# Optimization experiments

Hardware: AMD Instinct MI355X
Metric: run time of the kernel (lower is better)

## Reference

```python
import jax, jax.numpy as jnp
import numpy as np

DIM_X = 128
DIM_Z = 128
DIM_IN = DIM_X + DIM_Z   # LSTM units == input width in this model
UNITS = DIM_IN
BATCH = 256
SEQ_LEN = 1024


def setup_inputs() -> dict:
    key = jax.random.key(0)
    ks = jax.random.split(key, 9)
    s = 0.05
    inputs = jax.random.normal(ks[0], (BATCH, SEQ_LEN, DIM_X), jnp.float32)
    # Keras LSTMCell params: kernel [dim_in, 4*units], recurrent_kernel [units, 4*units], bias [4*units]
    kernel = jax.random.normal(ks[1], (DIM_IN, 4 * UNITS), jnp.float32) * s
    recurrent_kernel = jax.random.normal(ks[2], (UNITS, 4 * UNITS), jnp.float32) * s
    bias = jax.random.normal(ks[3], (4 * UNITS,), jnp.float32) * s
    # Gaussian heads
    w_mu = jax.random.normal(ks[4], (UNITS, DIM_Z), jnp.float32) * s
    b_mu = jnp.zeros((DIM_Z,), jnp.float32)
    w_sigma = jax.random.normal(ks[5], (UNITS, DIM_Z), jnp.float32) * s
    b_sigma = jnp.zeros((DIM_Z,), jnp.float32)
    eps = jax.random.normal(ks[6], (SEQ_LEN - 1, BATCH, DIM_Z), jnp.float32)
    return {"inputs": inputs, "kernel": kernel, "recurrent_kernel": recurrent_kernel,
            "bias": bias, "w_mu": w_mu, "b_mu": b_mu, "w_sigma": w_sigma,
            "b_sigma": b_sigma, "eps": eps}


def reference(inputs, kernel, recurrent_kernel, bias, w_mu, b_mu, w_sigma, b_sigma, eps):
    B = inputs.shape[0]

    def cell(h, c, zx):
        # Keras gate order: i, f, g(candidate), o
        gates = zx @ kernel + h @ recurrent_kernel + bias
        i, f, g, o = jnp.split(gates, 4, axis=-1)
        c = jax.nn.sigmoid(f) * c + jax.nn.sigmoid(i) * jnp.tanh(g)
        h = jax.nn.sigmoid(o) * jnp.tanh(c)
        return h, c

    def heads(h):
        mu = h @ w_mu + b_mu
        sigma = jax.nn.softplus(h @ w_sigma + b_sigma) + 1e-6
        return mu, sigma

    # warmup: z = zeros, x = inputs[:, 0, :], zero LSTM state
    h0 = jnp.zeros((B, UNITS), inputs.dtype)
    c0 = jnp.zeros((B, UNITS), inputs.dtype)
    z0 = jnp.zeros((B, DIM_Z), inputs.dtype)
    h, c = cell(h0, c0, jnp.concatenate([z0, inputs[:, 0, :]], axis=-1))
    mu0, sigma0 = heads(h)

    xs = (jnp.swapaxes(inputs[:, 1:, :], 0, 1), eps)  # [T-1, B, dim_x], [T-1, B, dim_z]

    def step(carry, x_eps):
        h, c, mu, sigma = carry
        x, e = x_eps
        z = mu + sigma * e  # reparameterized sample
        h, c = cell(h, c, jnp.concatenate([z, x], axis=-1))
        mu, sigma = heads(h)
        return (h, c, mu, sigma), (mu, sigma)

    _, (mus, sigmas) = jax.lax.scan(step, (h, c, mu0, sigma0), xs)
    mu_preds = jnp.swapaxes(jnp.concatenate([mu0[None], mus], axis=0), 0, 1)      # [B, T, dim_z]
    sigma_preds = jnp.swapaxes(jnp.concatenate([sigma0[None], sigmas], axis=0), 0, 1)
    return (mu_preds, sigma_preds)
```

## Files before the change

### kernel.cpp

```cpp
#include <hip/hip_runtime.h>
#include <hip/hip_bf16.h>
#include <math.h>


#define BATCH 256
#define SEQT  1024
#define DX    128
#define DZ    128
#define UNITS 256
#define G4    1024

__device__ __forceinline__ float ldf(const float* p) { return *p; }
__device__ __forceinline__ float ldf(const __hip_bfloat16* p) { return __bfloat162float(*p); }
__device__ __forceinline__ void stf(float* p, float v) { *p = v; }
__device__ __forceinline__ void stf(__hip_bfloat16* p, float v) { *p = __float2bfloat16(v); }

__device__ __forceinline__ float sigmoidf_(float x) { return 1.0f / (1.0f + expf(-x)); }
__device__ __forceinline__ float softplusf_(float x) {
    float ax = fabsf(x);
    return fmaxf(x, 0.0f) + log1pf(expf(-ax));
}

__global__ void detect_dtype_kernel(const unsigned short* __restrict__ bias_words,
                                    int* __restrict__ flag) {
    __shared__ int any_big;
    if (threadIdx.x == 0) any_big = 0;
    __syncthreads();
    int local = 0;
    for (int i = threadIdx.x; i < 1024; i += 256) {
        unsigned short w = bias_words[i];
        int e = (w >> 7) & 0xFF;
        if (e >= 127) local = 1;
    }
    if (local) atomicOr(&any_big, 1);
    __syncthreads();
    if (threadIdx.x == 0) flag[0] = any_big;
}

template <typename T>
__global__ __launch_bounds__(256) void lstm_ar_kernel(
    const int* __restrict__ flag, int want,
    const T* __restrict__ inp,
    const T* __restrict__ K,
    const T* __restrict__ R,
    const T* __restrict__ bias,
    const T* __restrict__ Wmu,
    const T* __restrict__ bmu,
    const T* __restrict__ Wsig,
    const T* __restrict__ bsig,
    const T* __restrict__ eps,
    T* __restrict__ out)
{
    if (flag[0] != want) return;

    const int b = blockIdx.x;
    const int u = threadIdx.x;

    __shared__ float zx_s[256];
    __shared__ float h_s[256];
    __shared__ float mu_s[128];
    __shared__ float sg_s[128];

    float c = 0.0f;

    const float b_i = ldf(bias + u);
    const float b_f = ldf(bias + 256 + u);
    const float b_g = ldf(bias + 512 + u);
    const float b_o = ldf(bias + 768 + u);
    const float b_head = (u < 128) ? ldf(bmu + u) : ldf(bsig + (u - 128));

    zx_s[u] = 0.0f;
    h_s[u] = 0.0f;
    __syncthreads();
    if (u < 128) {
        zx_s[128 + u] = ldf(inp + ((size_t)b * SEQT + 0) * DX + u);
    }
    __syncthreads();

    const size_t out_sig_off = (size_t)BATCH * SEQT * DZ;

    for (int t = 0; t < SEQT; ++t) {
        float ai = b_i, af = b_f, ag = b_g, ao = b_o;
        {
            const T* kp = K + u;
            #pragma unroll 8
            for (int i = 0; i < 256; ++i) {
                const float a = zx_s[i];
                ai += a * ldf(kp);
                af += a * ldf(kp + 256);
                ag += a * ldf(kp + 512);
                ao += a * ldf(kp + 768);
                kp += G4;
            }
        }
        {
            const T* rp = R + u;
            #pragma unroll 8
            for (int i = 0; i < 256; ++i) {
                const float a = h_s[i];
                ai += a * ldf(rp);
                af += a * ldf(rp + 256);
                ag += a * ldf(rp + 512);
                ao += a * ldf(rp + 768);
                rp += G4;
            }
        }

        const float gi = sigmoidf_(ai);
        const float gf = sigmoidf_(af);
        const float gg = tanhf(ag);
        const float go = sigmoidf_(ao);
        c = gf * c + gi * gg;
        const float hn = go * tanhf(c);

        __syncthreads();
        h_s[u] = hn;
        __syncthreads();

        float acc = b_head;
        if (u < 128) {
            const T* wp = Wmu + u;
            #pragma unroll 8
            for (int k = 0; k < 256; ++k) {
                acc += h_s[k] * ldf(wp);
                wp += DZ;
            }
            mu_s[u] = acc;
            stf(out + ((size_t)b * SEQT + t) * DZ + u, acc);
        } else {
            const int d = u - 128;
            const T* wp = Wsig + d;
            #pragma unroll 8
            for (int k = 0; k < 256; ++k) {
                acc += h_s[k] * ldf(wp);
                wp += DZ;
            }
            const float sg = softplusf_(acc) + 1e-6f;
            sg_s[d] = sg;
            stf(out + out_sig_off + ((size_t)b * SEQT + t) * DZ + d, sg);
        }
        __syncthreads();

        if (t < SEQT - 1) {
            if (u < 128) {
                const float e = ldf(eps + ((size_t)t * BATCH + b) * DZ + u);
                zx_s[u] = mu_s[u] + sg_s[u] * e;
                zx_s[128 + u] = ldf(inp + ((size_t)b * SEQT + (t + 1)) * DX + u);
            }
        }
        __syncthreads();
    }
}

template <typename T>
static void launch_main(const int* flag, int want, void* const* d_in, void* d_out,
                        hipStream_t stream) {
    lstm_ar_kernel<T><<<BATCH, 256, 0, stream>>>(
        flag, want,
        (const T*)d_in[0], (const T*)d_in[1], (const T*)d_in[2], (const T*)d_in[3],
        (const T*)d_in[4], (const T*)d_in[5], (const T*)d_in[6], (const T*)d_in[7],
        (const T*)d_in[8], (T*)d_out);
}

extern "C" void kernel_launch(void* const* d_in, const int* in_sizes, int n_in,
                              void* d_out, int out_size, void* d_ws, size_t ws_size,
                              hipStream_t stream) {
    int* flag = (int*)d_ws;
    detect_dtype_kernel<<<1, 256, 0, stream>>>((const unsigned short*)d_in[3], flag);
    launch_main<__hip_bfloat16>(flag, 0, d_in, d_out, stream);
    launch_main<float>(flag, 1, d_in, d_out, stream);
}
```

Baseline: 23.76 ms.

## Split LSTM weights across persistent blocks with LDS-resident slices and flag-based exchange

Replaces the one-block-per-batch-row kernel, which streamed all of K, R and the head weights from global memory every timestep, with a persistent cooperative grid of 256 blocks. Each block holds a 32-gate-column slice of K/R and an 8-column slice of the head weights in LDS, and serves 32 batch rows. Blocks trade h and z through global buffers and per-group atomic flags, so a spin-wait group barrier runs twice per timestep. This removes the repeated global weight traffic at the cost of grid-level synchronisation latency, and it depends on all blocks being co-resident.

Result: slower. 92.88 ms (+290.9%).

```diff
diff --git a/kernel.cpp b/kernel.cpp
--- a/kernel.cpp
+++ b/kernel.cpp
@@ -10,6 +10,25 @@
 #define UNITS 256
 #define G4    1024
 
+#define RG    8
+#define CBN   32
+#define MROWS 32
+#define UB    8
+#define NTHR  512
+
+#define ACT_STR 516
+
+#define WG_OFF    0
+#define WH_OFF    (WG_OFF + 512*32)
+#define ACT_OFF   (WH_OFF + 256*8)
+#define GRED_OFF  (ACT_OFF + MROWS*ACT_STR)
+#define HSCR_OFF  (GRED_OFF + 32*32)
+#define MUSIG_OFF (HSCR_OFF + 32*8)
+#define BG_OFF    (MUSIG_OFF + 32*8)
+#define BH_OFF    (BG_OFF + 32)
+#define LDS_FLOATS (BH_OFF + 8)
+#define LDS_BYTES  (LDS_FLOATS * 4)
+
 __device__ __forceinline__ float ldf(const float* p) { return *p; }
 __device__ __forceinline__ float ldf(const __hip_bfloat16* p) { return __bfloat162float(*p); }
 __device__ __forceinline__ void stf(float* p, float v) { *p = v; }
@@ -20,6 +39,12 @@
     float ax = fabsf(x);
     return fmaxf(x, 0.0f) + log1pf(expf(-ax));
 }
+
+__device__ float g_h_ex[2][RG][MROWS][UNITS];
+__device__ float g_z_ex[2][RG][MROWS][DZ];
+__device__ __align__(128) int g_flag_h[RG][CBN];
+__device__ __align__(128) int g_flag_z[RG][CBN];
+__device__ int g_abort;
 
 __global__ void detect_dtype_kernel(const unsigned short* __restrict__ bias_words,
                                     int* __restrict__ flag) {
@@ -37,8 +62,35 @@
     if (threadIdx.x == 0) flag[0] = any_big;
 }
 
+__global__ void reset_flags_kernel() {
+    int i = threadIdx.x;
+    if (i < RG * CBN) {
+        __hip_atomic_store(&(&g_flag_h[0][0])[i], -1, __ATOMIC_RELAXED, __HIP_MEMORY_SCOPE_AGENT);
+        __hip_atomic_store(&(&g_flag_z[0][0])[i], -1, __ATOMIC_RELAXED, __HIP_MEMORY_SCOPE_AGENT);
+    }
+    if (i == 0) __hip_atomic_store(&g_abort, 0, __ATOMIC_RELAXED, __HIP_MEMORY_SCOPE_AGENT);
+}
+
+__device__ __forceinline__ void wait_group_flags(int* fl, int tval, int tid) {
+    if (tid < CBN) {
+        int n = 0;
+        while (__hip_atomic_load(&fl[tid], __ATOMIC_RELAXED, __HIP_MEMORY_SCOPE_AGENT) < tval) {
+            __builtin_amdgcn_s_sleep(2);
+            if ((++n & 2047) == 0) {
+                if (__hip_atomic_load(&g_abort, __ATOMIC_RELAXED, __HIP_MEMORY_SCOPE_AGENT) != 0) break;
+                if (n > 8000000) {
+                    __hip_atomic_store(&g_abort, 1, __ATOMIC_RELAXED, __HIP_MEMORY_SCOPE_AGENT);
+                    break;
+                }
+            }
+        }
+    }
+    __builtin_amdgcn_fence(__ATOMIC_ACQUIRE, "agent");
+    __syncthreads();
+}
+
 template <typename T>
-__global__ __launch_bounds__(256) void lstm_ar_kernel(
+__global__ __launch_bounds__(NTHR, 1) void lstm_persist(
     const int* __restrict__ flag, int want,
     const T* __restrict__ inp,
     const T* __restrict__ K,
@@ -52,121 +104,221 @@
     T* __restrict__ out)
 {
     if (flag[0] != want) return;
-
-    const int b = blockIdx.x;
-    const int u = threadIdx.x;
-
-    __shared__ float zx_s[256];
-    __shared__ float h_s[256];
-    __shared__ float mu_s[128];
-    __shared__ float sg_s[128];
-
-    float c = 0.0f;
-
-    const float b_i = ldf(bias + u);
-    const float b_f = ldf(bias + 256 + u);
-    const float b_g = ldf(bias + 512 + u);
-    const float b_o = ldf(bias + 768 + u);
-    const float b_head = (u < 128) ? ldf(bmu + u) : ldf(bsig + (u - 128));
-
-    zx_s[u] = 0.0f;
-    h_s[u] = 0.0f;
-    __syncthreads();
-    if (u < 128) {
-        zx_s[128 + u] = ldf(inp + ((size_t)b * SEQT + 0) * DX + u);
-    }
-    __syncthreads();
-
-    const size_t out_sig_off = (size_t)BATCH * SEQT * DZ;
+    extern __shared__ float lds[];
+
+    const int tid = threadIdx.x;
+    const int rg  = blockIdx.x & (RG - 1);
+    const int cb  = blockIdx.x >> 3;
+    const int u0  = cb * UB;
+    const int z0  = cb * 4;
+
+    float* Wg    = lds + WG_OFF;
+    float* Wh    = lds + WH_OFF;
+    float* act   = lds + ACT_OFF;
+    float* gred  = lds + GRED_OFF;
+    float* hscr  = lds + HSCR_OFF;
+    float* musig = lds + MUSIG_OFF;
+    float* bg    = lds + BG_OFF;
+    float* bh    = lds + BH_OFF;
+
+    for (int idx = tid; idx < 512 * 32; idx += NTHR) {
+        int k = idx >> 5, c = idx & 31;
+        int col = ((c >> 3) << 8) + u0 + (c & 7);
+        float v = (k < 256) ? ldf(K + (size_t)k * G4 + col)
+                            : ldf(R + (size_t)(k - 256) * G4 + col);
+        Wg[k * 32 + c] = v;
+    }
+    for (int idx = tid; idx < 256 * 8; idx += NTHR) {
+        int k = idx >> 3, hc = idx & 7;
+        float v = (hc < 4) ? ldf(Wmu + (size_t)k * DZ + z0 + hc)
+                           : ldf(Wsig + (size_t)k * DZ + z0 + (hc - 4));
+        Wh[k * 8 + hc] = v;
+    }
+    if (tid < 32) bg[tid] = ldf(bias + ((tid >> 3) << 8) + u0 + (tid & 7));
+    if (tid < 8)  bh[tid] = (tid < 4) ? ldf(bmu + z0 + tid) : ldf(bsig + z0 + tid - 4);
+
+    for (int idx = tid; idx < MROWS * 512; idx += NTHR) {
+        int r = idx >> 9, c = idx & 511;
+        act[r * ACT_STR + c] = 0.0f;
+    }
+    __syncthreads();
+    {
+        int r = tid >> 4, j0 = (tid & 15) * 8;
+        const T* ip = inp + (size_t)(rg * MROWS + r) * SEQT * DX + j0;
+        float* dx = act + r * ACT_STR + 128 + j0;
+        #pragma unroll
+        for (int j = 0; j < 8; ++j) dx[j] = ldf(ip + j);
+    }
+    __syncthreads();
+
+    const int kh = tid >> 8;
+    const int gr = (tid >> 3) & 31;
+    const int cq = tid & 7;
+    const int kbase = kh * 256;
+
+    float cst = 0.0f;
+    const size_t OUT_SIG = (size_t)BATCH * SEQT * DZ;
 
     for (int t = 0; t < SEQT; ++t) {
-        float ai = b_i, af = b_f, ag = b_g, ao = b_o;
+        if (t > 0) {
+            wait_group_flags(g_flag_z[rg], t, tid);
+            int r = tid >> 4, j0 = (tid & 15) * 8;
+            const float* zp = &g_z_ex[t & 1][rg][r][j0];
+            float* dzp = act + r * ACT_STR + j0;
+            #pragma unroll
+            for (int j = 0; j < 8; ++j)
+                dzp[j] = __hip_atomic_load(zp + j, __ATOMIC_RELAXED, __HIP_MEMORY_SCOPE_AGENT);
+            __syncthreads();
+        }
+
+        float a0 = 0.f, a1 = 0.f, a2 = 0.f, a3 = 0.f;
         {
-            const T* kp = K + u;
-            #pragma unroll 8
-            for (int i = 0; i < 256; ++i) {
-                const float a = zx_s[i];
-                ai += a * ldf(kp);
-                af += a * ldf(kp + 256);
-                ag += a * ldf(kp + 512);
-                ao += a * ldf(kp + 768);
-                kp += G4;
-            }
-        }
+            const float* ap = act + gr * ACT_STR + kbase;
+            const float* wp = Wg + kbase * 32 + cq * 4;
+            #pragma unroll 2
+            for (int k = 0; k < 256; k += 4) {
+                float4 av = *(const float4*)(ap + k);
+                float4 w0 = *(const float4*)(wp + (k    ) * 32);
+                float4 w1 = *(const float4*)(wp + (k + 1) * 32);
+                float4 w2 = *(const float4*)(wp + (k + 2) * 32);
+                float4 w3 = *(const float4*)(wp + (k + 3) * 32);
+                a0 = fmaf(av.x, w0.x, a0); a1 = fmaf(av.x, w0.y, a1);
+                a2 = fmaf(av.x, w0.z, a2); a3 = fmaf(av.x, w0.w, a3);
+                a0 = fmaf(av.y, w1.x, a0); a1 = fmaf(av.y, w1.y, a1);
+                a2 = fmaf(av.y, w1.z, a2); a3 = fmaf(av.y, w1.w, a3);
+                a0 = fmaf(av.z, w2.x, a0); a1 = fmaf(av.z, w2.y, a1);
+                a2 = fmaf(av.z, w2.z, a2); a3 = fmaf(av.z, w2.w, a3);
+                a0 = fmaf(av.w, w3.x, a0); a1 = fmaf(av.w, w3.y, a1);
+                a2 = fmaf(av.w, w3.z, a2); a3 = fmaf(av.w, w3.w, a3);
+            }
+        }
+        if (kh == 1)
+            *(float4*)(gred + gr * 32 + cq * 4) = make_float4(a0, a1, a2, a3);
+        __syncthreads();
+        if (kh == 0) {
+            float4 p = *(const float4*)(gred + gr * 32 + cq * 4);
+            a0 += p.x + bg[cq * 4 + 0]; a1 += p.y + bg[cq * 4 + 1];
+            a2 += p.z + bg[cq * 4 + 2]; a3 += p.w + bg[cq * 4 + 3];
+            *(float4*)(gred + gr * 32 + cq * 4) = make_float4(a0, a1, a2, a3);
+        }
+        __syncthreads();
+
+        if (tid < 256) {
+            int r = tid >> 3, uu = tid & 7;
+            float gi = gred[r * 32 +      uu];
+            float gf = gred[r * 32 +  8 + uu];
+            float gg = gred[r * 32 + 16 + uu];
+            float go = gred[r * 32 + 24 + uu];
+            cst = sigmoidf_(gf) * cst + sigmoidf_(gi) * tanhf(gg);
+            float hn = sigmoidf_(go) * tanhf(cst);
+            __hip_atomic_store(&g_h_ex[t & 1][rg][r][u0 + uu], hn,
+                               __ATOMIC_RELAXED, __HIP_MEMORY_SCOPE_AGENT);
+        }
+        __builtin_amdgcn_fence(__ATOMIC_RELEASE, "agent");
+        __syncthreads();
+        if (tid == 0)
+            __hip_atomic_store(&g_flag_h[rg][cb], t, __ATOMIC_RELEASE, __HIP_MEMORY_SCOPE_AGENT);
+
+        wait_group_flags(g_flag_h[rg], t, tid);
         {
-            const T* rp = R + u;
-            #pragma unroll 8
-            for (int i = 0; i < 256; ++i) {
-                const float a = h_s[i];
-                ai += a * ldf(rp);
-                af += a * ldf(rp + 256);
-                ag += a * ldf(rp + 512);
-                ao += a * ldf(rp + 768);
-                rp += G4;
-            }
-        }
-
-        const float gi = sigmoidf_(ai);
-        const float gf = sigmoidf_(af);
-        const float gg = tanhf(ag);
-        const float go = sigmoidf_(ao);
-        c = gf * c + gi * gg;
-        const float hn = go * tanhf(c);
-
-        __syncthreads();
-        h_s[u] = hn;
-        __syncthreads();
-
-        float acc = b_head;
-        if (u < 128) {
-            const T* wp = Wmu + u;
-            #pragma unroll 8
-            for (int k = 0; k < 256; ++k) {
-                acc += h_s[k] * ldf(wp);
-                wp += DZ;
-            }
-            mu_s[u] = acc;
-            stf(out + ((size_t)b * SEQT + t) * DZ + u, acc);
-        } else {
-            const int d = u - 128;
-            const T* wp = Wsig + d;
-            #pragma unroll 8
-            for (int k = 0; k < 256; ++k) {
-                acc += h_s[k] * ldf(wp);
-                wp += DZ;
-            }
-            const float sg = softplusf_(acc) + 1e-6f;
-            sg_s[d] = sg;
-            stf(out + out_sig_off + ((size_t)b * SEQT + t) * DZ + d, sg);
-        }
-        __syncthreads();
-
-        if (t < SEQT - 1) {
-            if (u < 128) {
-                const float e = ldf(eps + ((size_t)t * BATCH + b) * DZ + u);
-                zx_s[u] = mu_s[u] + sg_s[u] * e;
-                zx_s[128 + u] = ldf(inp + ((size_t)b * SEQT + (t + 1)) * DX + u);
-            }
-        }
-        __syncthreads();
+            int r = tid >> 4, j0 = (tid & 15) * 16;
+            const float* hp = &g_h_ex[t & 1][rg][r][j0];
+            float* dh = act + r * ACT_STR + 256 + j0;
+            #pragma unroll
+            for (int j = 0; j < 16; ++j)
+                dh[j] = __hip_atomic_load(hp + j, __ATOMIC_RELAXED, __HIP_MEMORY_SCOPE_AGENT);
+            if (t + 1 < SEQT) {
+                int j0x = (tid & 15) * 8;
+                const T* ip = inp + ((size_t)(rg * MROWS + r) * SEQT + (t + 1)) * DX + j0x;
+                float* dx = act + r * ACT_STR + 128 + j0x;
+                #pragma unroll
+                for (int j = 0; j < 8; ++j) dx[j] = ldf(ip + j);
+            }
+        }
+        __syncthreads();
+
+        float hacc = 0.0f;
+        {
+            const int hc = tid & 7;
+            const float* ap = act + gr * ACT_STR + 256 + kh * 128;
+            const float* wp = Wh + (kh * 128) * 8 + hc;
+            #pragma unroll 4
+            for (int k = 0; k < 128; ++k)
+                hacc = fmaf(ap[k], wp[k * 8], hacc);
+        }
+        if (kh == 1) hscr[gr * 8 + (tid & 7)] = hacc;
+        __syncthreads();
+        if (kh == 0) {
+            int hc = tid & 7;
+            float tot = hacc + hscr[gr * 8 + hc] + bh[hc];
+            size_t ob = ((size_t)(rg * MROWS + gr) * SEQT + t) * DZ + z0;
+            if (hc < 4) {
+                musig[gr * 8 + hc] = tot;
+                stf(out + ob + hc, tot);
+            } else {
+                float sg = softplusf_(tot) + 1e-6f;
+                musig[gr * 8 + hc] = sg;
+                stf(out + OUT_SIG + ob + (hc - 4), sg);
+            }
+        }
+        __syncthreads();
+
+        if (t + 1 < SEQT) {
+            if (tid < 128) {
+                int r = tid >> 2, zc = tid & 3;
+                float mu = musig[r * 8 + zc];
+                float sg = musig[r * 8 + 4 + zc];
+                float e  = ldf(eps + ((size_t)t * BATCH + (rg * MROWS + r)) * DZ + z0 + zc);
+                float zv = fmaf(sg, e, mu);
+                __hip_atomic_store(&g_z_ex[(t + 1) & 1][rg][r][z0 + zc], zv,
+                                   __ATOMIC_RELAXED, __HIP_MEMORY_SCOPE_AGENT);
+            }
+            __builtin_amdgcn_fence(__ATOMIC_RELEASE, "agent");
+            __syncthreads();
+            if (tid == 0)
+                __hip_atomic_store(&g_flag_z[rg][cb], t + 1, __ATOMIC_RELEASE, __HIP_MEMORY_SCOPE_AGENT);
+        }
     }
 }
 
 template <typename T>
-static void launch_main(const int* flag, int want, void* const* d_in, void* d_out,
-                        hipStream_t stream) {
-    lstm_ar_kernel<T><<<BATCH, 256, 0, stream>>>(
-        flag, want,
-        (const T*)d_in[0], (const T*)d_in[1], (const T*)d_in[2], (const T*)d_in[3],
-        (const T*)d_in[4], (const T*)d_in[5], (const T*)d_in[6], (const T*)d_in[7],
-        (const T*)d_in[8], (T*)d_out);
+static void launch_persist(const int* flag, int want, void* const* d_in, void* d_out,
+                           hipStream_t stream) {
+    const T* a_inp  = (const T*)d_in[0];
+    const T* a_K    = (const T*)d_in[1];
+    const T* a_R    = (const T*)d_in[2];
+    const T* a_b    = (const T*)d_in[3];
+    const T* a_Wmu  = (const T*)d_in[4];
+    const T* a_bmu  = (const T*)d_in[5];
+    const T* a_Wsig = (const T*)d_in[6];
+    const T* a_bsig = (const T*)d_in[7];
+    const T* a_eps  = (const T*)d_in[8];
+    T* a_out = (T*)d_out;
+    const int* a_flag = flag;
+    int a_want = want;
+    void* args[] = { (void*)&a_flag, (void*)&a_want, (void*)&a_inp, (void*)&a_K,
+                     (void*)&a_R, (void*)&a_b, (void*)&a_Wmu, (void*)&a_bmu,
+                     (void*)&a_Wsig, (void*)&a_bsig, (void*)&a_eps, (void*)&a_out };
+    hipError_t e = hipLaunchCooperativeKernel((void*)(&lstm_persist<T>),
+                                              dim3(RG * CBN), dim3(NTHR),
+                                              args, LDS_BYTES, stream);
+    if (e != hipSuccess) {
+        lstm_persist<T><<<dim3(RG * CBN), dim3(NTHR), LDS_BYTES, stream>>>(
+            a_flag, a_want, a_inp, a_K, a_R, a_b, a_Wmu, a_bmu, a_Wsig, a_bsig,
+            a_eps, a_out);
+    }
 }
 
 extern "C" void kernel_launch(void* const* d_in, const int* in_sizes, int n_in,
                               void* d_out, int out_size, void* d_ws, size_t ws_size,
                               hipStream_t stream) {
     int* flag = (int*)d_ws;
+    hipFuncSetAttribute((const void*)(&lstm_persist<__hip_bfloat16>),
+                        hipFuncAttributeMaxDynamicSharedMemorySize, LDS_BYTES);
+    hipFuncSetAttribute((const void*)(&lstm_persist<float>),
+                        hipFuncAttributeMaxDynamicSharedMemorySize, LDS_BYTES);
     detect_dtype_kernel<<<1, 256, 0, stream>>>((const unsigned short*)d_in[3], flag);
-    launch_main<__hip_bfloat16>(flag, 0, d_in, d_out, stream);
-    launch_main<float>(flag, 1, d_in, d_out, stream);
-}
+    reset_flags_kernel<<<1, 256, 0, stream>>>();
+    launch_persist<__hip_bfloat16>(flag, 0, d_in, d_out, stream);
+    launch_persist<float>(flag, 1, d_in, d_out, stream);
+}
```

## Process four batch rows per block with split-K gate and head matmuls

Applied to the files above, without the earlier changes.

Each block now handles four batch rows with 1024 threads, so every weight element loaded from global/L2 is reused across four rows instead of one. The gate matmul is split so half the threads do the input kernel and half the recurrent kernel, reduced through shared memory; weights are loaded as paired columns and activations as float4. The head projection is split four ways over K and reduced, and the next step's eps/input values are prefetched at the top of the step. This reduces weight traffic per row but cuts the grid to 64 blocks and adds extra barriers per step.

Result: slower. 34.94 ms (+47.0%).

```diff
diff --git a/kernel.cpp b/kernel.cpp
--- a/kernel.cpp
+++ b/kernel.cpp
@@ -10,10 +10,22 @@
 #define UNITS 256
 #define G4    1024
 
+#define RPB   4
+#define NBLK  (BATCH / RPB)
+#define NTHR  1024
+
 __device__ __forceinline__ float ldf(const float* p) { return *p; }
 __device__ __forceinline__ float ldf(const __hip_bfloat16* p) { return __bfloat162float(*p); }
 __device__ __forceinline__ void stf(float* p, float v) { *p = v; }
 __device__ __forceinline__ void stf(__hip_bfloat16* p, float v) { *p = __float2bfloat16(v); }
+
+__device__ __forceinline__ float2 ld2(const float* p) { return *(const float2*)p; }
+__device__ __forceinline__ float2 ld2(const __hip_bfloat16* p) {
+    unsigned int u = *(const unsigned int*)p;
+    union { unsigned int i; float f; } a, b;
+    a.i = u << 16; b.i = u & 0xffff0000u;
+    return make_float2(a.f, b.f);
+}
 
 __device__ __forceinline__ float sigmoidf_(float x) { return 1.0f / (1.0f + expf(-x)); }
 __device__ __forceinline__ float softplusf_(float x) {
@@ -38,7 +50,7 @@
 }
 
 template <typename T>
-__global__ __launch_bounds__(256) void lstm_ar_kernel(
+__global__ __launch_bounds__(NTHR) void lstm_r4(
     const int* __restrict__ flag, int want,
     const T* __restrict__ inp,
     const T* __restrict__ K,
@@ -53,99 +65,160 @@
 {
     if (flag[0] != want) return;
 
-    const int b = blockIdx.x;
-    const int u = threadIdx.x;
-
-    __shared__ float zx_s[256];
-    __shared__ float h_s[256];
-    __shared__ float mu_s[128];
-    __shared__ float sg_s[128];
-
-    float c = 0.0f;
-
-    const float b_i = ldf(bias + u);
-    const float b_f = ldf(bias + 256 + u);
-    const float b_g = ldf(bias + 512 + u);
-    const float b_o = ldf(bias + 768 + u);
-    const float b_head = (u < 128) ? ldf(bmu + u) : ldf(bsig + (u - 128));
-
-    zx_s[u] = 0.0f;
-    h_s[u] = 0.0f;
-    __syncthreads();
-    if (u < 128) {
-        zx_s[128 + u] = ldf(inp + ((size_t)b * SEQT + 0) * DX + u);
+    __shared__ __align__(16) float act[RPB][516];
+    __shared__ __align__(16) float gred[RPB][1024];
+    __shared__ __align__(16) float hred[3][RPB][256];
+    __shared__ __align__(16) float mus[RPB][128];
+    __shared__ __align__(16) float sgs[RPB][128];
+
+    const int tid = threadIdx.x;
+    const int b0  = blockIdx.x * RPB;
+
+    const int q  = tid & 127;
+    const int g  = (tid >> 7) & 3;
+    const int kh = tid >> 9;
+    const int c0 = g * 256 + q * 2;
+    const T* wp0 = ((kh == 0) ? K : R) + c0;
+    const int acol0 = kh * 256;
+    float2 bg = make_float2(0.0f, 0.0f);
+    if (kh == 0) bg = ld2(bias + c0);
+
+    const int hc = tid & 255;
+    const int ks = tid >> 8;
+    const T* hw0 = (hc < 128) ? (Wmu  + (size_t)(ks * 64) * DZ + hc)
+                              : (Wsig + (size_t)(ks * 64) * DZ + (hc - 128));
+    float bh = 0.0f;
+    if (ks == 0) bh = (hc < 128) ? ldf(bmu + hc) : ldf(bsig + hc - 128);
+
+    const int cu = tid & 255;
+    const int cr = tid >> 8;
+    float cst = 0.0f;
+
+    for (int i = tid; i < RPB * 512; i += NTHR) act[i >> 9][i & 511] = 0.0f;
+    __syncthreads();
+    if (tid < 512) {
+        int r = tid >> 7, xc = tid & 127;
+        act[r][128 + xc] = ldf(inp + (size_t)(b0 + r) * SEQT * DX + xc);
     }
     __syncthreads();
 
-    const size_t out_sig_off = (size_t)BATCH * SEQT * DZ;
+    const size_t OUT_SIG = (size_t)BATCH * SEQT * DZ;
 
     for (int t = 0; t < SEQT; ++t) {
-        float ai = b_i, af = b_f, ag = b_g, ao = b_o;
+        float pf = 0.0f;
+        if (t + 1 < SEQT) {
+            if (tid < 512) {
+                int r = tid >> 7, zc = tid & 127;
+                pf = ldf(eps + ((size_t)t * BATCH + b0 + r) * DZ + zc);
+            } else {
+                int j = tid & 511, r = j >> 7, xc = j & 127;
+                pf = ldf(inp + ((size_t)(b0 + r) * SEQT + (t + 1)) * DX + xc);
+            }
+        }
+
+        float2 acc[RPB];
+        #pragma unroll
+        for (int r = 0; r < RPB; ++r) acc[r] = make_float2(0.0f, 0.0f);
         {
-            const T* kp = K + u;
-            #pragma unroll 8
-            for (int i = 0; i < 256; ++i) {
-                const float a = zx_s[i];
-                ai += a * ldf(kp);
-                af += a * ldf(kp + 256);
-                ag += a * ldf(kp + 512);
-                ao += a * ldf(kp + 768);
-                kp += G4;
-            }
-        }
+            const T* wp = wp0;
+            #pragma unroll 2
+            for (int k = 0; k < 256; k += 4) {
+                float2 w0 = ld2(wp);
+                float2 w1 = ld2(wp + G4);
+                float2 w2 = ld2(wp + 2 * G4);
+                float2 w3 = ld2(wp + 3 * G4);
+                wp += 4 * G4;
+                float4 a0 = *(const float4*)&act[0][acol0 + k];
+                float4 a1 = *(const float4*)&act[1][acol0 + k];
+                float4 a2 = *(const float4*)&act[2][acol0 + k];
+                float4 a3 = *(const float4*)&act[3][acol0 + k];
+                acc[0].x = fmaf(a0.x, w0.x, fmaf(a0.y, w1.x, fmaf(a0.z, w2.x, fmaf(a0.w, w3.x, acc[0].x))));
+                acc[0].y = fmaf(a0.x, w0.y, fmaf(a0.y, w1.y, fmaf(a0.z, w2.y, fmaf(a0.w, w3.y, acc[0].y))));
+                acc[1].x = fmaf(a1.x, w0.x, fmaf(a1.y, w1.x, fmaf(a1.z, w2.x, fmaf(a1.w, w3.x, acc[1].x))));
+                acc[1].y = fmaf(a1.x, w0.y, fmaf(a1.y, w1.y, fmaf(a1.z, w2.y, fmaf(a1.w, w3.y, acc[1].y))));
+                acc[2].x = fmaf(a2.x, w0.x, fmaf(a2.y, w1.x, fmaf(a2.z, w2.x, fmaf(a2.w, w3.x, acc[2].x))));
+                acc[2].y = fmaf(a2.x, w0.y, fmaf(a2.y, w1.y, fmaf(a2.z, w2.y, fmaf(a2.w, w3.y, acc[2].y))));
+                acc[3].x = fmaf(a3.x, w0.x, fmaf(a3.y, w1.x, fmaf(a3.z, w2.x, fmaf(a3.w, w3.x, acc[3].x))));
+                acc[3].y = fmaf(a3.x, w0.y, fmaf(a3.y, w1.y, fmaf(a3.z, w2.y, fmaf(a3.w, w3.y, acc[3].y))));
+            }
+        }
+        if (kh == 1) {
+            #pragma unroll
+            for (int r = 0; r < RPB; ++r)
+                *(float2*)&gred[r][c0] = acc[r];
+        }
+        __syncthreads();
+        if (kh == 0) {
+            #pragma unroll
+            for (int r = 0; r < RPB; ++r) {
+                float2 p = *(const float2*)&gred[r][c0];
+                p.x += acc[r].x + bg.x;
+                p.y += acc[r].y + bg.y;
+                *(float2*)&gred[r][c0] = p;
+            }
+        }
+        __syncthreads();
+
         {
-            const T* rp = R + u;
-            #pragma unroll 8
-            for (int i = 0; i < 256; ++i) {
-                const float a = h_s[i];
-                ai += a * ldf(rp);
-                af += a * ldf(rp + 256);
-                ag += a * ldf(rp + 512);
-                ao += a * ldf(rp + 768);
-                rp += G4;
-            }
-        }
-
-        const float gi = sigmoidf_(ai);
-        const float gf = sigmoidf_(af);
-        const float gg = tanhf(ag);
-        const float go = sigmoidf_(ao);
-        c = gf * c + gi * gg;
-        const float hn = go * tanhf(c);
-
-        __syncthreads();
-        h_s[u] = hn;
-        __syncthreads();
-
-        float acc = b_head;
-        if (u < 128) {
-            const T* wp = Wmu + u;
-            #pragma unroll 8
-            for (int k = 0; k < 256; ++k) {
-                acc += h_s[k] * ldf(wp);
-                wp += DZ;
-            }
-            mu_s[u] = acc;
-            stf(out + ((size_t)b * SEQT + t) * DZ + u, acc);
-        } else {
-            const int d = u - 128;
-            const T* wp = Wsig + d;
-            #pragma unroll 8
-            for (int k = 0; k < 256; ++k) {
-                acc += h_s[k] * ldf(wp);
-                wp += DZ;
-            }
-            const float sg = softplusf_(acc) + 1e-6f;
-            sg_s[d] = sg;
-            stf(out + out_sig_off + ((size_t)b * SEQT + t) * DZ + d, sg);
-        }
-        __syncthreads();
-
-        if (t < SEQT - 1) {
-            if (u < 128) {
-                const float e = ldf(eps + ((size_t)t * BATCH + b) * DZ + u);
-                zx_s[u] = mu_s[u] + sg_s[u] * e;
-                zx_s[128 + u] = ldf(inp + ((size_t)b * SEQT + (t + 1)) * DX + u);
+            float gi = gred[cr][cu];
+            float gf = gred[cr][256 + cu];
+            float gg = gred[cr][512 + cu];
+            float go = gred[cr][768 + cu];
+            cst = sigmoidf_(gf) * cst + sigmoidf_(gi) * tanhf(gg);
+            act[cr][256 + cu] = sigmoidf_(go) * tanhf(cst);
+        }
+        __syncthreads();
+
+        float hacc[RPB] = {0.0f, 0.0f, 0.0f, 0.0f};
+        {
+            const T* hw = hw0;
+            const int a0c = 256 + ks * 64;
+            #pragma unroll 2
+            for (int kk = 0; kk < 64; kk += 4) {
+                float w0 = ldf(hw);
+                float w1 = ldf(hw + DZ);
+                float w2 = ldf(hw + 2 * DZ);
+                float w3 = ldf(hw + 3 * DZ);
+                hw += 4 * DZ;
+                float4 a0 = *(const float4*)&act[0][a0c + kk];
+                float4 a1 = *(const float4*)&act[1][a0c + kk];
+                float4 a2 = *(const float4*)&act[2][a0c + kk];
+                float4 a3 = *(const float4*)&act[3][a0c + kk];
+                hacc[0] = fmaf(a0.x, w0, fmaf(a0.y, w1, fmaf(a0.z, w2, fmaf(a0.w, w3, hacc[0]))));
+                hacc[1] = fmaf(a1.x, w0, fmaf(a1.y, w1, fmaf(a1.z, w2, fmaf(a1.w, w3, hacc[1]))));
+                hacc[2] = fmaf(a2.x, w0, fmaf(a2.y, w1, fmaf(a2.z, w2, fmaf(a2.w, w3, hacc[2]))));
+                hacc[3] = fmaf(a3.x, w0, fmaf(a3.y, w1, fmaf(a3.z, w2, fmaf(a3.w, w3, hacc[3]))));
+            }
+        }
+        if (ks >= 1) {
+            #pragma unroll
+            for (int r = 0; r < RPB; ++r) hred[ks - 1][r][hc] = hacc[r];
+        }
+        __syncthreads();
+        if (ks == 0) {
+            #pragma unroll
+            for (int r = 0; r < RPB; ++r) {
+                float tot = hacc[r] + hred[0][r][hc] + hred[1][r][hc] + hred[2][r][hc] + bh;
+                size_t ob = ((size_t)(b0 + r) * SEQT + t) * DZ;
+                if (hc < 128) {
+                    mus[r][hc] = tot;
+                    stf(out + ob + hc, tot);
+                } else {
+                    float sg = softplusf_(tot) + 1e-6f;
+                    sgs[r][hc - 128] = sg;
+                    stf(out + OUT_SIG + ob + (hc - 128), sg);
+                }
+            }
+        }
+        __syncthreads();
+
+        if (t + 1 < SEQT) {
+            if (tid < 512) {
+                int r = tid >> 7, zc = tid & 127;
+                act[r][zc] = fmaf(sgs[r][zc], pf, mus[r][zc]);
+            } else {
+                int j = tid & 511, r = j >> 7, xc = j & 127;
+                act[r][128 + xc] = pf;
             }
         }
         __syncthreads();
@@ -155,7 +228,7 @@
 template <typename T>
 static void launch_main(const int* flag, int want, void* const* d_in, void* d_out,
                         hipStream_t stream) {
-    lstm_ar_kernel<T><<<BATCH, 256, 0, stream>>>(
+    lstm_r4<T><<<NBLK, NTHR, 0, stream>>>(
         flag, want,
         (const T*)d_in[0], (const T*)d_in[1], (const T*)d_in[2], (const T*)d_in[3],
         (const T*)d_in[4], (const T*)d_in[5], (const T*)d_in[6], (const T*)d_in[7],
```

## Split LSTM gate matvec across 1024 threads with K-split reduction and paired loads

Applied to the files above, without the earlier changes.

Moves the per-batch block from 256 to 1024 threads. The gate matvec is split so half the threads handle the input kernel and half the recurrent kernel, each computing two adjacent columns with paired loads and float4 activation reads, and the two partial sums are reduced through shared memory. The Gaussian heads are split 8 ways along K with a shared-memory reduction, and next-step eps and input loads are prefetched at the top of each step. This targets the serial per-thread dot-product latency, at the cost of more barriers and shared memory per step.

Result: slower. 30.87 ms (+29.9%).

```diff
diff --git a/kernel.cpp b/kernel.cpp
--- a/kernel.cpp
+++ b/kernel.cpp
@@ -9,11 +9,20 @@
 #define DZ    128
 #define UNITS 256
 #define G4    1024
+#define NTHR  1024
 
 __device__ __forceinline__ float ldf(const float* p) { return *p; }
 __device__ __forceinline__ float ldf(const __hip_bfloat16* p) { return __bfloat162float(*p); }
 __device__ __forceinline__ void stf(float* p, float v) { *p = v; }
 __device__ __forceinline__ void stf(__hip_bfloat16* p, float v) { *p = __float2bfloat16(v); }
+
+__device__ __forceinline__ float2 ldpair(const float* p) { return *(const float2*)p; }
+__device__ __forceinline__ float2 ldpair(const __hip_bfloat16* p) {
+    unsigned int u = *(const unsigned int*)p;
+    union { unsigned int i; float f; } a, b;
+    a.i = u << 16; b.i = u & 0xffff0000u;
+    return make_float2(a.f, b.f);
+}
 
 __device__ __forceinline__ float sigmoidf_(float x) { return 1.0f / (1.0f + expf(-x)); }
 __device__ __forceinline__ float softplusf_(float x) {
@@ -38,11 +47,11 @@
 }
 
 template <typename T>
-__global__ __launch_bounds__(256) void lstm_ar_kernel(
+__global__ __launch_bounds__(NTHR) void lstm_r1(
     const int* __restrict__ flag, int want,
     const T* __restrict__ inp,
     const T* __restrict__ K,
-    const T* __restrict__ R,
+    const T* __restrict__ Rw,
     const T* __restrict__ bias,
     const T* __restrict__ Wmu,
     const T* __restrict__ bmu,
@@ -53,109 +62,135 @@
 {
     if (flag[0] != want) return;
 
-    const int b = blockIdx.x;
-    const int u = threadIdx.x;
-
-    __shared__ float zx_s[256];
-    __shared__ float h_s[256];
-    __shared__ float mu_s[128];
-    __shared__ float sg_s[128];
-
-    float c = 0.0f;
-
-    const float b_i = ldf(bias + u);
-    const float b_f = ldf(bias + 256 + u);
-    const float b_g = ldf(bias + 512 + u);
-    const float b_o = ldf(bias + 768 + u);
-    const float b_head = (u < 128) ? ldf(bmu + u) : ldf(bsig + (u - 128));
-
-    zx_s[u] = 0.0f;
-    h_s[u] = 0.0f;
-    __syncthreads();
-    if (u < 128) {
-        zx_s[128 + u] = ldf(inp + ((size_t)b * SEQT + 0) * DX + u);
+    __shared__ __align__(16) float act[512];
+    __shared__ __align__(16) float gA[1024];
+    __shared__ __align__(16) float gB[1024];
+    __shared__ __align__(16) float hred[8][256];
+    __shared__ __align__(16) float mus[128];
+    __shared__ __align__(16) float sgs[128];
+
+    const int tid = threadIdx.x;
+    const int b   = blockIdx.x;
+
+    const int cp = tid & 511;
+    const int kh = tid >> 9;
+    const T* wp0 = ((kh == 0) ? K : Rw) + 2 * cp;
+    const float* actp = act + kh * 256;
+
+    const int cp2 = tid & 127;
+    const int ks  = tid >> 7;
+    const T* hw0 = (cp2 < 64) ? (Wmu + 2 * cp2) : (Wsig + 2 * cp2 - 128);
+    hw0 += (size_t)(32 * ks) * DZ;
+
+    float b_i = 0.f, b_f = 0.f, b_g = 0.f, b_o = 0.f, bh = 0.f;
+    if (tid < 256) {
+        b_i = ldf(bias + tid);
+        b_f = ldf(bias + 256 + tid);
+        b_g = ldf(bias + 512 + tid);
+        b_o = ldf(bias + 768 + tid);
+        bh  = (tid < 128) ? ldf(bmu + tid) : ldf(bsig + tid - 128);
     }
-    __syncthreads();
-
-    const size_t out_sig_off = (size_t)BATCH * SEQT * DZ;
+    float cst = 0.0f;
+
+    const T* inpp = inp + (size_t)b * SEQT * DX;
+    const T* epsp = eps + (size_t)b * DZ;
+    T* outmu = out + (size_t)b * SEQT * DZ;
+    T* outsg = outmu + (size_t)BATCH * SEQT * DZ;
+
+    if (tid < 512) act[tid] = 0.0f;
+    __syncthreads();
+    if (tid < 128) act[128 + tid] = ldf(inpp + tid);
+    __syncthreads();
 
     for (int t = 0; t < SEQT; ++t) {
-        float ai = b_i, af = b_f, ag = b_g, ao = b_o;
+        float pf = 0.0f;
+        if (t + 1 < SEQT) {
+            if (tid < 128)       pf = ldf(epsp + tid);
+            else if (tid < 256)  pf = ldf(inpp + DX + (tid - 128));
+        }
+
+        float2 acc = make_float2(0.0f, 0.0f);
         {
-            const T* kp = K + u;
-            #pragma unroll 8
-            for (int i = 0; i < 256; ++i) {
-                const float a = zx_s[i];
-                ai += a * ldf(kp);
-                af += a * ldf(kp + 256);
-                ag += a * ldf(kp + 512);
-                ao += a * ldf(kp + 768);
-                kp += G4;
+            const T* wp = wp0;
+            #pragma unroll 2
+            for (int k0 = 0; k0 < 256; k0 += 4) {
+                float4 av = *(const float4*)(actp + k0);
+                float2 w0 = ldpair(wp);
+                float2 w1 = ldpair(wp + G4);
+                float2 w2 = ldpair(wp + 2 * G4);
+                float2 w3 = ldpair(wp + 3 * G4);
+                wp += 4 * G4;
+                acc.x = fmaf(av.x, w0.x, fmaf(av.y, w1.x, fmaf(av.z, w2.x, fmaf(av.w, w3.x, acc.x))));
+                acc.y = fmaf(av.x, w0.y, fmaf(av.y, w1.y, fmaf(av.z, w2.y, fmaf(av.w, w3.y, acc.y))));
             }
         }
         {
-            const T* rp = R + u;
-            #pragma unroll 8
-            for (int i = 0; i < 256; ++i) {
-                const float a = h_s[i];
-                ai += a * ldf(rp);
-                af += a * ldf(rp + 256);
-                ag += a * ldf(rp + 512);
-                ao += a * ldf(rp + 768);
-                rp += G4;
+            float* gdst = kh ? gB : gA;
+            *(float2*)&gdst[2 * cp] = acc;
+        }
+        __syncthreads();
+
+        if (tid < 256) {
+            float ai = gA[tid]       + gB[tid]       + b_i;
+            float af = gA[256 + tid] + gB[256 + tid] + b_f;
+            float ag = gA[512 + tid] + gB[512 + tid] + b_g;
+            float ao = gA[768 + tid] + gB[768 + tid] + b_o;
+            cst = sigmoidf_(af) * cst + sigmoidf_(ai) * tanhf(ag);
+            act[256 + tid] = sigmoidf_(ao) * tanhf(cst);
+        }
+        __syncthreads();
+
+        float2 hacc = make_float2(0.0f, 0.0f);
+        {
+            const float* hap = act + 256 + 32 * ks;
+            const T* hw = hw0;
+            #pragma unroll
+            for (int k0 = 0; k0 < 32; k0 += 4) {
+                float4 av = *(const float4*)(hap + k0);
+                float2 w0 = ldpair(hw);
+                float2 w1 = ldpair(hw + DZ);
+                float2 w2 = ldpair(hw + 2 * DZ);
+                float2 w3 = ldpair(hw + 3 * DZ);
+                hw += 4 * DZ;
+                hacc.x = fmaf(av.x, w0.x, fmaf(av.y, w1.x, fmaf(av.z, w2.x, fmaf(av.w, w3.x, hacc.x))));
+                hacc.y = fmaf(av.x, w0.y, fmaf(av.y, w1.y, fmaf(av.z, w2.y, fmaf(av.w, w3.y, hacc.y))));
             }
         }
-
-        const float gi = sigmoidf_(ai);
-        const float gf = sigmoidf_(af);
-        const float gg = tanhf(ag);
-        const float go = sigmoidf_(ao);
-        c = gf * c + gi * gg;
-        const float hn = go * tanhf(c);
-
-        __syncthreads();
-        h_s[u] = hn;
-        __syncthreads();
-
-        float acc = b_head;
-        if (u < 128) {
-            const T* wp = Wmu + u;
-            #pragma unroll 8
-            for (int k = 0; k < 256; ++k) {
-                acc += h_s[k] * ldf(wp);
-                wp += DZ;
+        *(float2*)&hred[ks][2 * cp2] = hacc;
+        __syncthreads();
+
+        if (tid < 256) {
+            float tot = bh;
+            #pragma unroll
+            for (int s = 0; s < 8; ++s) tot += hred[s][tid];
+            if (tid < 128) {
+                mus[tid] = tot;
+                stf(outmu + tid, tot);
+            } else {
+                float sg = softplusf_(tot) + 1e-6f;
+                sgs[tid - 128] = sg;
+                stf(outsg + (tid - 128), sg);
             }
-            mu_s[u] = acc;
-            stf(out + ((size_t)b * SEQT + t) * DZ + u, acc);
-        } else {
-            const int d = u - 128;
-            const T* wp = Wsig + d;
-            #pragma unroll 8
-            for (int k = 0; k < 256; ++k) {
-                acc += h_s[k] * ldf(wp);
-                wp += DZ;
-            }
-            const float sg = softplusf_(acc) + 1e-6f;
-            sg_s[d] = sg;
-            stf(out + out_sig_off + ((size_t)b * SEQT + t) * DZ + d, sg);
-        }
-        __syncthreads();
-
-        if (t < SEQT - 1) {
-            if (u < 128) {
-                const float e = ldf(eps + ((size_t)t * BATCH + b) * DZ + u);
-                zx_s[u] = mu_s[u] + sg_s[u] * e;
-                zx_s[128 + u] = ldf(inp + ((size_t)b * SEQT + (t + 1)) * DX + u);
-            }
-        }
-        __syncthreads();
+        }
+        __syncthreads();
+
+        if (t + 1 < SEQT) {
+            if (tid < 128)       act[tid] = fmaf(sgs[tid], pf, mus[tid]);
+            else if (tid < 256)  act[128 + (tid - 128)] = pf;
+        }
+        __syncthreads();
+
+        inpp  += DX;
+        epsp  += (size_t)BATCH * DZ;
+        outmu += DZ;
+        outsg += DZ;
     }
 }
 
 template <typename T>
 static void launch_main(const int* flag, int want, void* const* d_in, void* d_out,
                         hipStream_t stream) {
-    lstm_ar_kernel<T><<<BATCH, 256, 0, stream>>>(
+    lstm_r1<T><<<BATCH, NTHR, 0, stream>>>(
         flag, want,
         (const T*)d_in[0], (const T*)d_in[1], (const T*)d_in[2], (const T*)d_in[3],
         (const T*)d_in[4], (const T*)d_in[5], (const T*)d_in[6], (const T*)d_in[7],
```
